# Kernel tuning notes

Hardware: AMD Instinct MI355X
Metric: run time of the kernel (lower is better)

## Reference

```python
import jax, jax.numpy as jnp
import numpy as np

B, L = 1024, 64          # sentences, tokens per sentence
V, E = 100000, 300       # vocab, embedding dim
RH, M, NC = 50, 50, 3    # rnn_hidden, mem_dim, num_class
N = B * L                # total tree nodes


def setup_inputs() -> dict:
    key = jax.random.key(0)
    ks = jax.random.split(key, 24)
    rn = lambda k, s, sc=0.05: jax.random.normal(k, s, dtype=jnp.float32) * sc
    # balanced binary dependency tree per sentence: parent(i) = (i-1)//2
    loc = np.arange(L)
    par_loc = np.where(loc == 0, -1, (loc - 1) // 2)
    parent = np.where(par_loc[None, :] < 0, -1,
                      par_loc[None, :] + np.arange(B)[:, None] * L).reshape(-1)
    depth = np.tile(np.floor(np.log2(loc + 1)).astype(np.int64), B)
    tm = np.zeros(L, np.float32); tm[1:4] = 1.0  # 3 aspect-target tokens/sentence
    return {
        "embed_ids": jax.random.randint(ks[0], (B, L), 0, V),
        "parent": jnp.asarray(parent),
        "depth": jnp.asarray(depth),
        "target_mask": jnp.asarray(np.tile(tm, B)),
        "num_levels": 7,
        "embed_table": rn(ks[1], (V, E), 1.0),
        "W_ih_f": rn(ks[2], (4 * RH, E)), "W_hh_f": rn(ks[3], (4 * RH, RH)),
        "b_f": rn(ks[4], (4 * RH,)),
        "W_ih_b": rn(ks[5], (4 * RH, E)), "W_hh_b": rn(ks[6], (4 * RH, RH)),
        "b_b": rn(ks[7], (4 * RH,)),
        "W_iou": rn(ks[8], (3 * M, 2 * RH)),
        "U_iou_w": rn(ks[9], (3 * M, M)), "U_iou_b": rn(ks[10], (3 * M,)),
        "b_iou": jnp.zeros((3 * M,), jnp.float32),
        "U_f_w": rn(ks[11], (M, M)), "U_f_b": rn(ks[12], (M,)),
        "H_w": rn(ks[13], (M, 2 * RH)), "H_b": rn(ks[14], (M,)),
        "C_w": rn(ks[15], (NC, M)), "C_b": rn(ks[16], (NC,)),
    }


def _lstm(x, W_ih, W_hh, b, reverse):
    # x: (B, L, E) -> (B, L, H); PyTorch gate order i, f, g, o
    xg = jnp.einsum('ble,ge->blg', x, W_ih) + b
    H = W_hh.shape[1]
    def step(carry, xt):
        h, c = carry
        g = xt + h @ W_hh.T
        i, f, gg, o = jnp.split(g, 4, axis=-1)
        c = jax.nn.sigmoid(f) * c + jax.nn.sigmoid(i) * jnp.tanh(gg)
        h = jax.nn.sigmoid(o) * jnp.tanh(c)
        return (h, c), h
    z = jnp.zeros((x.shape[0], H), x.dtype)
    _, hs = jax.lax.scan(step, (z, z), jnp.swapaxes(xg, 0, 1), reverse=reverse)
    return jnp.swapaxes(hs, 0, 1)


def reference(embed_ids, parent, depth, target_mask, num_levels, embed_table,
              W_ih_f, W_hh_f, b_f, W_ih_b, W_hh_b, b_b,
              W_iou, U_iou_w, U_iou_b, b_iou, U_f_w, U_f_b,
              H_w, H_b, C_w, C_b):
    # --- BiLSTM encoder (dropout = identity at inference) ---
    emb = embed_table[embed_ids]                       # (B,L,E) gather
    hf = _lstm(emb, W_ih_f, W_hh_f, b_f, False)
    hb = _lstm(emb, W_ih_b, W_hh_b, b_b, True)
    x = jnp.concatenate([hf, hb], -1).reshape(N, 2 * RH)
    # --- ChildSum TreeLSTM, topological (deepest level first) ---
    iou0 = x @ W_iou.T                                 # (N, 3M)
    h_init = x @ H_w.T + H_b                           # (N, M)
    parent_safe = jnp.where(parent >= 0, parent, N)    # roots -> dummy slot N
    counts = jnp.zeros(N + 1, jnp.int32).at[parent_safe].add(1)
    has_children = (counts[:N] > 0)[:, None]
    h_fin = h_init
    c_fin = jnp.zeros((N, M), jnp.float32)
    h_sum = jnp.zeros((N + 1, M), jnp.float32)         # sum of child h
    fc_sum = jnp.zeros((N + 1, M), jnp.float32)        # sum of f * child c
    for lvl in range(num_levels - 1, -1, -1):
        m = (depth == lvl)[:, None]
        # reduce: leaves never get U_iou bias (no mailbox in DGL)
        iou = iou0 + jnp.where(has_children, h_sum[:N] @ U_iou_w.T + U_iou_b, 0.0) + b_iou
        i, o, u = jnp.split(iou, 3, axis=-1)
        c_new = jax.nn.sigmoid(i) * jnp.tanh(u) + fc_sum[:N]
        h_new = h_init + jax.nn.sigmoid(o) * jnp.tanh(c_new)
        h_fin = jnp.where(m, h_new, h_fin)
        c_fin = jnp.where(m, c_new, c_fin)
        # scatter messages from this level's nodes to their parents
        f = jax.nn.sigmoid(h_new @ U_f_w.T + U_f_b)
        h_sum = h_sum.at[parent_safe].add(jnp.where(m, h_new, 0.0))
        fc_sum = fc_sum.at[parent_safe].add(jnp.where(m, f * c_new, 0.0))
    # --- masked mean pool over target tokens per sentence ---
    tm = target_mask.reshape(B, L)
    pooled = (h_fin.reshape(B, L, M) * tm[:, :, None]).sum(1) / tm.sum(1, keepdims=True)
    logits = pooled @ C_w.T + C_b
    return logits, pooled
```

## Files before the change

kernel.cpp:

```cpp
#include <hip/hip_runtime.h>


typedef __attribute__((ext_vector_type(8))) short bf16x8;
typedef __attribute__((ext_vector_type(4))) float f32x4;

__device__ __forceinline__ float fsig(float x) { return 1.0f / (1.0f + __expf(-x)); }
__device__ __forceinline__ float ftanh(float x) {
    float a = fabsf(x);
    float t = __expf(2.0f * a);
    float r = 1.0f - 2.0f / (t + 1.0f);
    return copysignf(r, x);
}
__device__ __forceinline__ float fsig2(float x) {
    float e = __builtin_amdgcn_exp2f(-1.4426950408889634f * x);
    return __builtin_amdgcn_rcpf(1.0f + e);
}
__device__ __forceinline__ float ftanh2(float x) {
    float e = __builtin_amdgcn_exp2f(2.8853900817779268f * x);
    return 1.0f - 2.0f * __builtin_amdgcn_rcpf(1.0f + e);
}

__device__ __forceinline__ unsigned short rne_bf16(float f) {
    unsigned u = __builtin_bit_cast(unsigned, f);
    unsigned r = u + 0x7fffu + ((u >> 16) & 1u);
    return (unsigned short)(r >> 16);
}
__device__ __forceinline__ void split2(float f, unsigned short& h, unsigned short& l) {
    h = rne_bf16(f);
    float fh = __builtin_bit_cast(float, ((unsigned)h) << 16);
    float r = f - fh;
    l = rne_bf16(r);
}

__device__ __forceinline__ void async_lds16(const void* g, void* l) {
    __builtin_amdgcn_global_load_lds(
        (const __attribute__((address_space(1))) unsigned int*)g,
        (__attribute__((address_space(3))) unsigned int*)l, 16, 0, 0);
}

__device__ __forceinline__ bf16x8 pack8(const unsigned short* h) {
    bf16x8 v;
    #pragma unroll
    for (int e = 0; e < 8; ++e) v[e] = (short)h[e];
    return v;
}

__global__ void conv_kernel(const float* __restrict__ B1, const float* __restrict__ B2,
                            int split, int K, int Rreal, int BN, int KCH,
                            unsigned short* __restrict__ out) {
    int q = blockIdx.x * 256 + threadIdx.x;
    int total = KCH * 4 * BN;
    if (q >= total) return;
    int n  = q % BN;
    int kq = (q / BN) & 3;
    int c  = q / (BN * 4);
    const float* row = (n < split) ? (B1 + (size_t)n * K) : (B2 + (size_t)(n - split) * K);
    unsigned short h[8], l[8];
    #pragma unroll
    for (int e = 0; e < 8; ++e) {
        int k = c * 32 + kq * 8 + e;
        float v = (n < Rreal && k < K) ? row[k] : 0.0f;
        split2(v, h[e], l[e]);
    }
    size_t hb = ((((size_t)c * 2 + 0) * 4 + kq) * BN + n) * 8;
    size_t lb = ((((size_t)c * 2 + 1) * 4 + kq) * BN + n) * 8;
    *(ushort4*)&out[hb]     = make_ushort4(h[0], h[1], h[2], h[3]);
    *(ushort4*)&out[hb + 4] = make_ushort4(h[4], h[5], h[6], h[7]);
    *(ushort4*)&out[lb]     = make_ushort4(l[0], l[1], l[2], l[3]);
    *(ushort4*)&out[lb + 4] = make_ushort4(l[4], l[5], l[6], l[7]);
}

template<int BN, int KCH, int KREAL, int NCOLS, bool GATHER>
__global__ __launch_bounds__(256, 2)
void gemm_split(const float* __restrict__ A, const int* __restrict__ ids,
                const unsigned short* __restrict__ Bc,
                const float* __restrict__ bias1, const float* __restrict__ bias2,
                int split, float* __restrict__ C) {
    constexpr int NTW = BN / 64;
    const int tid = threadIdx.x;
    const int m0 = blockIdx.x * 64;
    const int w = tid >> 6, lane = tid & 63;
    const int r16 = lane & 15, quad = lane >> 4;
    const int wn = w * (BN / 4);

    const float* arow[4];
    #pragma unroll
    for (int i = 0; i < 4; ++i) {
        int m = i * 16 + r16;
        arow[i] = GATHER ? (A + (size_t)ids[m0 + m] * KREAL)
                         : (A + (size_t)(m0 + m) * KREAL);
    }

    float ar[4][8];
    auto loadA = [&](int c) {
        const int k0 = c * 32 + quad * 8;
        #pragma unroll
        for (int i = 0; i < 4; ++i) {
            if (k0 + 8 <= KREAL) {
                float4 p = *(const float4*)(arow[i] + k0);
                float4 q = *(const float4*)(arow[i] + k0 + 4);
                ar[i][0]=p.x; ar[i][1]=p.y; ar[i][2]=p.z; ar[i][3]=p.w;
                ar[i][4]=q.x; ar[i][5]=q.y; ar[i][6]=q.z; ar[i][7]=q.w;
            } else {
                #pragma unroll
                for (int e = 0; e < 8; ++e)
                    ar[i][e] = (k0 + e < KREAL) ? arow[i][k0 + e] : 0.0f;
            }
        }
    };

    f32x4 acc[4][NTW] = {};
    loadA(0);

    #pragma unroll 1
    for (int c = 0; c < KCH; ++c) {
        bf16x8 ah[4], al[4];
        #pragma unroll
        for (int i = 0; i < 4; ++i) {
            unsigned short hh[8], ll[8];
            #pragma unroll
            for (int e = 0; e < 8; ++e) split2(ar[i][e], hh[e], ll[e]);
            ah[i] = pack8(hh);
            al[i] = pack8(ll);
        }
        if (c + 1 < KCH) loadA(c + 1);

        const unsigned short* bh_base = Bc + (size_t)((c * 2 + 0) * 4 + quad) * BN * 8;
        const unsigned short* bl_base = Bc + (size_t)((c * 2 + 1) * 4 + quad) * BN * 8;
        #pragma unroll
        for (int t = 0; t < NTW; ++t) {
            int n = wn + t * 16 + r16;
            bf16x8 bh = *(const bf16x8*)&bh_base[(size_t)n * 8];
            bf16x8 bl = *(const bf16x8*)&bl_base[(size_t)n * 8];
            #pragma unroll
            for (int i = 0; i < 4; ++i) {
                acc[i][t] = __builtin_amdgcn_mfma_f32_16x16x32_bf16(ah[i], bh, acc[i][t], 0, 0, 0);
                acc[i][t] = __builtin_amdgcn_mfma_f32_16x16x32_bf16(al[i], bh, acc[i][t], 0, 0, 0);
                acc[i][t] = __builtin_amdgcn_mfma_f32_16x16x32_bf16(ah[i], bl, acc[i][t], 0, 0, 0);
            }
        }
    }

    #pragma unroll
    for (int t = 0; t < NTW; ++t) {
        int ncol = wn + t * 16 + r16;
        if (ncol < NCOLS) {
            float bv = (ncol < split) ? bias1[ncol] : bias2[ncol - split];
            #pragma unroll
            for (int i = 0; i < 4; ++i)
                #pragma unroll
                for (int r = 0; r < 4; ++r) {
                    int mrow = m0 + i * 16 + quad * 4 + r;
                    C[(size_t)mrow * NCOLS + ncol] = acc[i][t][r] + bv;
                }
        }
    }
}

constexpr int WHC_DIR = 2 * 2 * 4 * 208 * 8;

__global__ __launch_bounds__(256)
void lstm_mfma(const float* __restrict__ xg, const unsigned short* __restrict__ Whc,
               float* __restrict__ x) {
    const int bi = blockIdx.x;
    const int dir = bi & 1;
    const int b0 = (bi >> 1) * 16;
    const int tid = threadIdx.x;
    const int w = tid >> 6, lane = tid & 63;
    const int r16 = lane & 15, quad = lane >> 4;

    __shared__ __align__(16) unsigned short Ah[8 * 16 * 8];
    __shared__ __align__(16) unsigned short Al[8 * 16 * 8];
    __shared__ __align__(16) float G[208 * 20];
    __shared__ __align__(16) float Xs[3][16][268];

    const int n0 = (w == 0) ? 0 : (w == 1) ? 4 : (w == 2) ? 7 : 10;
    const int nc = (w == 0) ? 4 : 3;

    const unsigned short* Wd = Whc + (size_t)dir * WHC_DIR;
    bf16x8 bfr[4][2][2];
    #pragma unroll
    for (int t = 0; t < 4; ++t) {
        int col = (n0 + ((t < nc) ? t : 0)) * 16 + r16;
        #pragma unroll
        for (int c = 0; c < 2; ++c)
            #pragma unroll
            for (int h = 0; h < 2; ++h)
                bfr[t][c][h] = *(const bf16x8*)&Wd[((((size_t)c * 2 + h) * 4 + quad) * 208 + col) * 8];
    }

    for (int q = tid; q < 512; q += 256) {
        ((unsigned*)Ah)[q] = 0u;
        ((unsigned*)Al)[q] = 0u;
    }

    int ss[4], ms[4];
    bool act[4];
    #pragma unroll
    for (int j = 0; j < 4; ++j) {
        int q = w * 200 + lane + 64 * j;
        ss[j] = q & 15;
        ms[j] = q >> 4;
        act[j] = (lane + 64 * j) < 200;
    }
    float c_reg[4] = {0.0f, 0.0f, 0.0f, 0.0f};

    #pragma unroll
    for (int p = 0; p < 2; ++p) {
        int idx0 = dir ? (63 - p) : p;
        #pragma unroll
        for (int i = 0; i < 4; ++i) {
            int s = w * 4 + i;
            const float* src = xg + ((size_t)(b0 + s) * 64 + idx0) * 400 + dir * 200 + lane * 4;
            async_lds16(src, &Xs[p][s][lane * 4]);
        }
    }
    __syncthreads();

    for (int step = 0; step < 64; ++step) {
        const int buf = step % 3;
        const int idx = dir ? (63 - step) : step;
        {
            int stepn = step + 2; if (stepn > 63) stepn = 63;
            const int slot = (step + 2) % 3;
            const int idxn = dir ? (63 - stepn) : stepn;
            #pragma unroll
            for (int i = 0; i < 4; ++i) {
                int s = w * 4 + i;
                const float* src = xg + ((size_t)(b0 + s) * 64 + idxn) * 400 + dir * 200 + lane * 4;
                async_lds16(src, &Xs[slot][s][lane * 4]);
            }
            __builtin_amdgcn_sched_barrier(0);
        }
        bf16x8 ah[2], al[2];
        #pragma unroll
        for (int c = 0; c < 2; ++c) {
            ah[c] = *(const bf16x8*)&Ah[((c * 4 + quad) * 16 + r16) * 8];
            al[c] = *(const bf16x8*)&Al[((c * 4 + quad) * 16 + r16) * 8];
        }
        f32x4 acc[4] = {};
        #pragma unroll
        for (int t = 0; t < 4; ++t) {
            if (t < nc) {
                #pragma unroll
                for (int c = 0; c < 2; ++c) {
                    acc[t] = __builtin_amdgcn_mfma_f32_16x16x32_bf16(ah[c], bfr[t][c][0], acc[t], 0, 0, 0);
                    acc[t] = __builtin_amdgcn_mfma_f32_16x16x32_bf16(al[c], bfr[t][c][0], acc[t], 0, 0, 0);
                    acc[t] = __builtin_amdgcn_mfma_f32_16x16x32_bf16(ah[c], bfr[t][c][1], acc[t], 0, 0, 0);
                }
            }
        }
        #pragma unroll
        for (int t = 0; t < 4; ++t) {
            if (t < nc) {
                int col = (n0 + t) * 16 + r16;
                *(f32x4*)&G[col * 20 + quad * 4] = acc[t];
            }
        }
        asm volatile("s_waitcnt lgkmcnt(0) vmcnt(16)" ::: "memory");
        __builtin_amdgcn_sched_barrier(0);
        __builtin_amdgcn_s_barrier();
        __builtin_amdgcn_sched_barrier(0);
        #pragma unroll
        for (int j = 0; j < 4; ++j) {
            if (act[j]) {
                int s = ss[j], m = ms[j];
                float gi = G[m * 20 + s]         + Xs[buf][s][m];
                float gf = G[(m + 50) * 20 + s]  + Xs[buf][s][m + 50];
                float gg = G[(m + 100) * 20 + s] + Xs[buf][s][m + 100];
                float go = G[(m + 150) * 20 + s] + Xs[buf][s][m + 150];
                c_reg[j] = fsig2(gf) * c_reg[j] + fsig2(gi) * ftanh2(gg);
                float h = fsig2(go) * ftanh2(c_reg[j]);
                unsigned short hh, hl;
                split2(h, hh, hl);
                Ah[(m >> 3) * 128 + s * 8 + (m & 7)] = hh;
                Al[(m >> 3) * 128 + s * 8 + (m & 7)] = hl;
                x[((size_t)(b0 + s) * 64 + idx) * 100 + dir * 50 + m] = h;
            }
        }
        asm volatile("s_waitcnt lgkmcnt(0)" ::: "memory");
        __builtin_amdgcn_sched_barrier(0);
        __builtin_amdgcn_s_barrier();
        __builtin_amdgcn_sched_barrier(0);
    }
}

__global__ __launch_bounds__(256)
void tree_kernel(const float* __restrict__ C2,
                 const float* __restrict__ Uw, const float* __restrict__ Ub,
                 const float* __restrict__ Fw, const float* __restrict__ Fb,
                 const float* __restrict__ tmask,
                 const float* __restrict__ Cw, const float* __restrict__ Cb,
                 float* __restrict__ out) {
    const int b = blockIdx.x;
    const int tid = threadIdx.x;

    __shared__ __align__(16) float h_sum[32][52];
    __shared__ __align__(16) float fc_sum[32][52];
    __shared__ __align__(16) float hcur[32][52];
    __shared__ __align__(16) float mcur[32][52];
    __shared__ float msg[16][152];
    __shared__ float hfin[64][50];
    __shared__ float pool[52];

    const int rU = (tid < 150) ? tid : 0;
    const int rF = tid % 50;
    float ur[50], fr[50];
    #pragma unroll
    for (int k = 0; k < 50; ++k) ur[k] = Uw[rU * 50 + k];
    #pragma unroll
    for (int k = 0; k < 50; ++k) fr[k] = Fw[rF * 50 + k];
    const float ub = Ub[rU];
    const float fb = Fb[rF];

    for (int q = tid; q < 32 * 52; q += 256) {
        h_sum[q / 52][q % 52] = 0.0f;
        fc_sum[q / 52][q % 52] = 0.0f;
    }
    __syncthreads();

    const float* c2b = C2 + (size_t)b * 64 * 200;

    for (int lvl = 6; lvl >= 0; --lvl) {
        const int lo = (1 << lvl) - 1;
        const int hi = min((1 << (lvl + 1)) - 2, 63);
        const int A = hi - lo + 1;
        const int chn = max(0, min(hi, 31) - lo + 1);

        if (tid < 150) {
            for (int a = 0; a < chn; ++a) {
                float acc = ub;
                #pragma unroll
                for (int k4 = 0; k4 < 12; ++k4) {
                    float4 h4 = *(const float4*)&h_sum[lo + a][k4 * 4];
                    acc += ur[k4*4+0]*h4.x + ur[k4*4+1]*h4.y + ur[k4*4+2]*h4.z + ur[k4*4+3]*h4.w;
                }
                acc += ur[48]*h_sum[lo + a][48] + ur[49]*h_sum[lo + a][49];
                msg[a][tid] = acc;
            }
        }
        __syncthreads();

        for (int q = tid; q < A * 50; q += 256) {
            int a = q / 50, m = q - a * 50;
            int loc = lo + a;
            const float* base = c2b + (size_t)loc * 200;
            bool ch = (a < chn);
            float ig = base[m]       + (ch ? msg[a][m]       : 0.0f);
            float og = base[50 + m]  + (ch ? msg[a][50 + m]  : 0.0f);
            float ug = base[100 + m] + (ch ? msg[a][100 + m] : 0.0f);
            float cn = fsig(ig) * ftanh(ug) + (ch ? fc_sum[loc][m] : 0.0f);
            float hn = base[150 + m] + fsig(og) * ftanh(cn);
            hcur[a][m] = hn;
            mcur[a][m] = cn;
            hfin[loc][m] = hn;
        }
        __syncthreads();

        if (tid < 250) {
            for (int a = tid / 50; a < A; a += 5) {
                float acc = fb;
                #pragma unroll
                for (int k4 = 0; k4 < 12; ++k4) {
                    float4 h4 = *(const float4*)&hcur[a][k4 * 4];
                    acc += fr[k4*4+0]*h4.x + fr[k4*4+1]*h4.y + fr[k4*4+2]*h4.z + fr[k4*4+3]*h4.w;
                }
                acc += fr[48]*hcur[a][48] + fr[49]*hcur[a][49];
                mcur[a][rF] = fsig(acc) * mcur[a][rF];
            }
        }
        __syncthreads();

        if (lvl > 0) {
            const int plo = (lo - 1) >> 1, phi = (hi - 1) >> 1;
            const int P = phi - plo + 1;
            for (int q = tid; q < P * 50; q += 256) {
                int pi = q / 50, m = q - pi * 50;
                int p = plo + pi;
                int c1 = 2 * p + 1, c2i = 2 * p + 2;
                float hs = hcur[c1 - lo][m];
                float fs = mcur[c1 - lo][m];
                if (c2i <= hi) { hs += hcur[c2i - lo][m]; fs += mcur[c2i - lo][m]; }
                h_sum[p][m] += hs;
                fc_sum[p][m] += fs;
            }
        }
        __syncthreads();
    }

    const float* tm = tmask + (size_t)b * 64;
    if (tid < 50) {
        float acc = 0.0f, ws = 0.0f;
        for (int l = 0; l < 64; ++l) {
            float wv = tm[l];
            ws += wv;
            acc += wv * hfin[l][tid];
        }
        float p = acc / ws;
        pool[tid] = p;
        out[3072 + (size_t)b * 50 + tid] = p;
    }
    __syncthreads();
    if (tid < 3) {
        float acc = Cb[tid];
        #pragma unroll
        for (int m = 0; m < 50; ++m) acc += Cw[tid * 50 + m] * pool[m];
        out[(size_t)b * 3 + tid] = acc;
    }
}

extern "C" void kernel_launch(void* const* d_in, const int* in_sizes, int n_in,
                              void* d_out, int out_size, void* d_ws, size_t ws_size,
                              hipStream_t stream) {
    (void)in_sizes; (void)n_in; (void)out_size; (void)ws_size;
    const int*   ids   = (const int*)d_in[0];
    const float* tmask = (const float*)d_in[3];
    const float* table = (const float*)d_in[5];
    const float* Wihf  = (const float*)d_in[6];
    const float* Whhf  = (const float*)d_in[7];
    const float* bf    = (const float*)d_in[8];
    const float* Wihb  = (const float*)d_in[9];
    const float* Whhb  = (const float*)d_in[10];
    const float* bb    = (const float*)d_in[11];
    const float* Wiou  = (const float*)d_in[12];
    const float* Uiouw = (const float*)d_in[13];
    const float* Uioub = (const float*)d_in[14];
    const float* biou  = (const float*)d_in[15];
    const float* Ufw   = (const float*)d_in[16];
    const float* Ufb   = (const float*)d_in[17];
    const float* Hw    = (const float*)d_in[18];
    const float* Hb    = (const float*)d_in[19];
    const float* Cw    = (const float*)d_in[20];
    const float* Cb    = (const float*)d_in[21];
    float* out = (float*)d_out;

    float* wsf = (float*)d_ws;
    float* xg = wsf;
    float* x  = wsf + (size_t)65536 * 400;
    float* C2 = wsf;
    unsigned short* B1c = (unsigned short*)(wsf + 32768000);
    unsigned short* B3c = (unsigned short*)(wsf + 32911360);
    unsigned short* Whc = (unsigned short*)(wsf + 32944128);

    conv_kernel<<<70, 256, 0, stream>>>(Wihf, Wihb, 200, 300, 400, 448, 10, B1c);
    conv_kernel<<<16, 256, 0, stream>>>(Wiou, Hw, 150, 100, 200, 256, 4, B3c);
    conv_kernel<<<7, 256, 0, stream>>>(Whhf, Whhf, 200, 50, 200, 208, 2, Whc);
    conv_kernel<<<7, 256, 0, stream>>>(Whhb, Whhb, 200, 50, 200, 208, 2, Whc + WHC_DIR);
    gemm_split<448, 10, 300, 400, true><<<1024, 256, 0, stream>>>(
        table, ids, B1c, bf, bb, 200, xg);
    lstm_mfma<<<128, 256, 0, stream>>>(xg, Whc, x);
    gemm_split<256, 4, 100, 200, false><<<1024, 256, 0, stream>>>(
        x, nullptr, B3c, biou, Hb, 150, C2);
    tree_kernel<<<1024, 256, 0, stream>>>(
        C2, Uiouw, Uioub, Ufw, Ufb, tmask, Cw, Cb, out);
}
```

Before: 494.7 us.

## Pipeline split-bf16 GEMMs with async LDS staging of B and column-half blocks

Replaces the split-bf16 GEMM kernel with a version that splits the output columns into two halves, each handled by its own block, doubling the grid. Each B chunk is staged into double-buffered LDS with async global-to-LDS loads, and the next A chunk is prefetched while MFMAs run on the current one. Each wave now owns 16 rows instead of all 64, so B reuse across row tiles moves from registers to LDS. The goal is to hide global B latency and raise occupancy and parallelism. The cost is more LDS use, a barrier per K-chunk, and A gather rows reloaded by both column-half blocks.

```diff
diff --git a/kernel.cpp b/kernel.cpp
--- a/kernel.cpp
+++ b/kernel.cpp
@@ -46,7 +46,7 @@
 }
 
 __global__ void conv_kernel(const float* __restrict__ B1, const float* __restrict__ B2,
-                            int split, int K, int Rreal, int BN, int KCH,
+                            int split, int K, int Rreal, int BN, int KCH, int n0,
                             unsigned short* __restrict__ out) {
     int q = blockIdx.x * 256 + threadIdx.x;
     int total = KCH * 4 * BN;
@@ -54,12 +54,13 @@
     int n  = q % BN;
     int kq = (q / BN) & 3;
     int c  = q / (BN * 4);
-    const float* row = (n < split) ? (B1 + (size_t)n * K) : (B2 + (size_t)(n - split) * K);
+    int ng = n0 + n;
+    const float* row = (ng < split) ? (B1 + (size_t)ng * K) : (B2 + (size_t)(ng - split) * K);
     unsigned short h[8], l[8];
     #pragma unroll
     for (int e = 0; e < 8; ++e) {
         int k = c * 32 + kq * 8 + e;
-        float v = (n < Rreal && k < K) ? row[k] : 0.0f;
+        float v = (ng < Rreal && k < K) ? row[k] : 0.0f;
         split2(v, h[e], l[e]);
     }
     size_t hb = ((((size_t)c * 2 + 0) * 4 + kq) * BN + n) * 8;
@@ -72,87 +73,106 @@
 
 template<int BN, int KCH, int KREAL, int NCOLS, bool GATHER>
 __global__ __launch_bounds__(256, 2)
-void gemm_split(const float* __restrict__ A, const int* __restrict__ ids,
-                const unsigned short* __restrict__ Bc,
-                const float* __restrict__ bias1, const float* __restrict__ bias2,
-                int split, float* __restrict__ C) {
-    constexpr int NTW = BN / 64;
+void gemm_pipe(const float* __restrict__ A, const int* __restrict__ ids,
+               const unsigned short* __restrict__ Bc0,
+               const unsigned short* __restrict__ Bc1,
+               const float* __restrict__ bias1, const float* __restrict__ bias2,
+               int split, float* __restrict__ C) {
+    static_assert(KREAL % 8 == 4, "tail fixup assumes KREAL%8==4");
+    static_assert(KCH % 2 == 0, "paired steps");
+    constexpr int NTW = BN / 16;
+    constexpr int CHB = 64 * BN;
+    constexpr int DMA_PT = CHB / 2048;
+    __shared__ __align__(16) unsigned short Bt[2][CHB];
+
     const int tid = threadIdx.x;
-    const int m0 = blockIdx.x * 64;
+    const int cb = blockIdx.x & 1;
+    const int m0 = (blockIdx.x >> 1) * 64;
     const int w = tid >> 6, lane = tid & 63;
     const int r16 = lane & 15, quad = lane >> 4;
-    const int wn = w * (BN / 4);
-
-    const float* arow[4];
-    #pragma unroll
-    for (int i = 0; i < 4; ++i) {
-        int m = i * 16 + r16;
-        arow[i] = GATHER ? (A + (size_t)ids[m0 + m] * KREAL)
-                         : (A + (size_t)(m0 + m) * KREAL);
-    }
-
-    float ar[4][8];
-    auto loadA = [&](int c) {
-        const int k0 = c * 32 + quad * 8;
-        #pragma unroll
-        for (int i = 0; i < 4; ++i) {
-            if (k0 + 8 <= KREAL) {
-                float4 p = *(const float4*)(arow[i] + k0);
-                float4 q = *(const float4*)(arow[i] + k0 + 4);
-                ar[i][0]=p.x; ar[i][1]=p.y; ar[i][2]=p.z; ar[i][3]=p.w;
-                ar[i][4]=q.x; ar[i][5]=q.y; ar[i][6]=q.z; ar[i][7]=q.w;
-            } else {
-                #pragma unroll
-                for (int e = 0; e < 8; ++e)
-                    ar[i][e] = (k0 + e < KREAL) ? arow[i][k0 + e] : 0.0f;
-            }
-        }
+    const int k0b = quad * 8;
+
+    const unsigned short* Bc = cb ? Bc1 : Bc0;
+    const int myrow = w * 16 + r16;
+    const float* arow = GATHER ? (A + (size_t)ids[m0 + myrow] * KREAL)
+                               : (A + (size_t)(m0 + myrow) * KREAL);
+
+    auto stageB = [&](int c, int slot) {
+        int cc = (c < KCH) ? c : (KCH - 1);
+        const unsigned short* src = Bc + (size_t)cc * CHB + tid * 8;
+        unsigned short* dst = &Bt[slot][tid * 8];
+        #pragma unroll
+        for (int i = 0; i < DMA_PT; ++i)
+            async_lds16(src + i * 2048, dst + i * 2048);
     };
-
-    f32x4 acc[4][NTW] = {};
-    loadA(0);
+    auto issueA = [&](int c, float4& p, float4& q) {
+        int k0 = c * 32 + k0b;
+        const float* src = arow + ((k0 <= KREAL - 8) ? k0 : (KREAL - 8));
+        p = *(const float4*)src;
+        q = *(const float4*)(src + 4);
+    };
+
+    f32x4 acc[NTW] = {};
+
+    auto step = [&](int c, float4& cp, float4& cq, float4& np, float4& nq) {
+        asm volatile("s_waitcnt lgkmcnt(0) vmcnt(2)" ::: "memory");
+        __builtin_amdgcn_sched_barrier(0);
+        __builtin_amdgcn_s_barrier();
+        __builtin_amdgcn_sched_barrier(0);
+        stageB(c + 1, (c + 1) & 1);
+        __builtin_amdgcn_sched_barrier(0);
+        issueA(c + 1, np, nq);
+        __builtin_amdgcn_sched_barrier(0);
+        float ar[8];
+        int k0 = c * 32 + k0b;
+        if (k0 <= KREAL - 8) {
+            ar[0]=cp.x; ar[1]=cp.y; ar[2]=cp.z; ar[3]=cp.w;
+            ar[4]=cq.x; ar[5]=cq.y; ar[6]=cq.z; ar[7]=cq.w;
+        } else {
+            float qq0 = cq.x, qq1 = cq.y, qq2 = cq.z, qq3 = cq.w;
+            ar[0] = (k0 + 0 < KREAL) ? qq0 : 0.0f;
+            ar[1] = (k0 + 1 < KREAL) ? qq1 : 0.0f;
+            ar[2] = (k0 + 2 < KREAL) ? qq2 : 0.0f;
+            ar[3] = (k0 + 3 < KREAL) ? qq3 : 0.0f;
+            ar[4] = 0.0f; ar[5] = 0.0f; ar[6] = 0.0f; ar[7] = 0.0f;
+        }
+        unsigned short hh[8], ll[8];
+        #pragma unroll
+        for (int e = 0; e < 8; ++e) split2(ar[e], hh[e], ll[e]);
+        bf16x8 ah = pack8(hh), al = pack8(ll);
+        const unsigned short* bb = &Bt[c & 1][0];
+        #pragma unroll
+        for (int t = 0; t < NTW; ++t) {
+            bf16x8 bh = *(const bf16x8*)&bb[((0 * 4 + quad) * BN + t * 16 + r16) * 8];
+            bf16x8 bl = *(const bf16x8*)&bb[((1 * 4 + quad) * BN + t * 16 + r16) * 8];
+            acc[t] = __builtin_amdgcn_mfma_f32_16x16x32_bf16(ah, bh, acc[t], 0, 0, 0);
+            acc[t] = __builtin_amdgcn_mfma_f32_16x16x32_bf16(al, bh, acc[t], 0, 0, 0);
+            acc[t] = __builtin_amdgcn_mfma_f32_16x16x32_bf16(ah, bl, acc[t], 0, 0, 0);
+        }
+    };
+
+    float4 pA, qA, pB, qB;
+    stageB(0, 0);
+    __builtin_amdgcn_sched_barrier(0);
+    issueA(0, pA, qA);
+    __builtin_amdgcn_sched_barrier(0);
 
     #pragma unroll 1
-    for (int c = 0; c < KCH; ++c) {
-        bf16x8 ah[4], al[4];
-        #pragma unroll
-        for (int i = 0; i < 4; ++i) {
-            unsigned short hh[8], ll[8];
-            #pragma unroll
-            for (int e = 0; e < 8; ++e) split2(ar[i][e], hh[e], ll[e]);
-            ah[i] = pack8(hh);
-            al[i] = pack8(ll);
-        }
-        if (c + 1 < KCH) loadA(c + 1);
-
-        const unsigned short* bh_base = Bc + (size_t)((c * 2 + 0) * 4 + quad) * BN * 8;
-        const unsigned short* bl_base = Bc + (size_t)((c * 2 + 1) * 4 + quad) * BN * 8;
-        #pragma unroll
-        for (int t = 0; t < NTW; ++t) {
-            int n = wn + t * 16 + r16;
-            bf16x8 bh = *(const bf16x8*)&bh_base[(size_t)n * 8];
-            bf16x8 bl = *(const bf16x8*)&bl_base[(size_t)n * 8];
-            #pragma unroll
-            for (int i = 0; i < 4; ++i) {
-                acc[i][t] = __builtin_amdgcn_mfma_f32_16x16x32_bf16(ah[i], bh, acc[i][t], 0, 0, 0);
-                acc[i][t] = __builtin_amdgcn_mfma_f32_16x16x32_bf16(al[i], bh, acc[i][t], 0, 0, 0);
-                acc[i][t] = __builtin_amdgcn_mfma_f32_16x16x32_bf16(ah[i], bl, acc[i][t], 0, 0, 0);
-            }
-        }
+    for (int c2 = 0; c2 < KCH / 2; ++c2) {
+        step(2 * c2,     pA, qA, pB, qB);
+        step(2 * c2 + 1, pB, qB, pA, qA);
     }
 
     #pragma unroll
     for (int t = 0; t < NTW; ++t) {
-        int ncol = wn + t * 16 + r16;
+        int ncol = cb * BN + t * 16 + r16;
         if (ncol < NCOLS) {
             float bv = (ncol < split) ? bias1[ncol] : bias2[ncol - split];
             #pragma unroll
-            for (int i = 0; i < 4; ++i)
-                #pragma unroll
-                for (int r = 0; r < 4; ++r) {
-                    int mrow = m0 + i * 16 + quad * 4 + r;
-                    C[(size_t)mrow * NCOLS + ncol] = acc[i][t][r] + bv;
-                }
+            for (int r = 0; r < 4; ++r) {
+                int mrow = m0 + w * 16 + quad * 4 + r;
+                C[(size_t)mrow * NCOLS + ncol] = acc[t][r] + bv;
+            }
         }
     }
 }
@@ -438,19 +458,23 @@
     float* xg = wsf;
     float* x  = wsf + (size_t)65536 * 400;
     float* C2 = wsf;
-    unsigned short* B1c = (unsigned short*)(wsf + 32768000);
-    unsigned short* B3c = (unsigned short*)(wsf + 32911360);
-    unsigned short* Whc = (unsigned short*)(wsf + 32944128);
-
-    conv_kernel<<<70, 256, 0, stream>>>(Wihf, Wihb, 200, 300, 400, 448, 10, B1c);
-    conv_kernel<<<16, 256, 0, stream>>>(Wiou, Hw, 150, 100, 200, 256, 4, B3c);
-    conv_kernel<<<7, 256, 0, stream>>>(Whhf, Whhf, 200, 50, 200, 208, 2, Whc);
-    conv_kernel<<<7, 256, 0, stream>>>(Whhb, Whhb, 200, 50, 200, 208, 2, Whc + WHC_DIR);
-    gemm_split<448, 10, 300, 400, true><<<1024, 256, 0, stream>>>(
-        table, ids, B1c, bf, bb, 200, xg);
+    unsigned short* B1cA = (unsigned short*)(wsf + 32768000);
+    unsigned short* B1cB = (unsigned short*)(wsf + 32839680);
+    unsigned short* B3cA = (unsigned short*)(wsf + 32911360);
+    unsigned short* B3cB = (unsigned short*)(wsf + 32927744);
+    unsigned short* Whc  = (unsigned short*)(wsf + 32944128);
+
+    conv_kernel<<<35, 256, 0, stream>>>(Wihf, Wihb, 200, 300, 400, 224, 10,   0, B1cA);
+    conv_kernel<<<35, 256, 0, stream>>>(Wihf, Wihb, 200, 300, 400, 224, 10, 224, B1cB);
+    conv_kernel<<< 8, 256, 0, stream>>>(Wiou, Hw,   150, 100, 200, 128,  4,   0, B3cA);
+    conv_kernel<<< 8, 256, 0, stream>>>(Wiou, Hw,   150, 100, 200, 128,  4, 128, B3cB);
+    conv_kernel<<< 7, 256, 0, stream>>>(Whhf, Whhf, 200,  50, 200, 208,  2,   0, Whc);
+    conv_kernel<<< 7, 256, 0, stream>>>(Whhb, Whhb, 200,  50, 200, 208,  2,   0, Whc + WHC_DIR);
+    gemm_pipe<224, 10, 300, 400, true><<<2048, 256, 0, stream>>>(
+        table, ids, B1cA, B1cB, bf, bb, 200, xg);
     lstm_mfma<<<128, 256, 0, stream>>>(xg, Whc, x);
-    gemm_split<256, 4, 100, 200, false><<<1024, 256, 0, stream>>>(
-        x, nullptr, B3c, biou, Hb, 150, C2);
+    gemm_pipe<128, 4, 100, 200, false><<<2048, 256, 0, stream>>>(
+        x, nullptr, B3cA, B3cB, biou, Hb, 150, C2);
     tree_kernel<<<1024, 256, 0, stream>>>(
         C2, Uiouw, Uioub, Ufw, Ufb, tmask, Cw, Cb, out);
 }
```

Result: faster. 475.7 us (-3.9%).
